# Kernel tuning notes

Hardware: AMD Instinct MI355X
Metric: run time of the kernel (lower is better)

The kernel has to match this reference:

```python
import jax, jax.numpy as jnp
import numpy as np

B, SQ, FDIM = 32, 196, 2048
L, EDIM, H = 1000, 1024, 16
DH = EDIM // H  # 64


def setup_inputs() -> dict:
    key = jax.random.key(0)
    ks = jax.random.split(key, 10)
    s = lambda fan_in: 1.0 / np.sqrt(fan_in)
    return {
        "features": jax.random.normal(ks[0], (B, SQ, FDIM), jnp.float32),
        "label_embeddings": jax.random.normal(ks[1], (L, EDIM), jnp.float32),
        "Wq": jax.random.normal(ks[2], (EDIM, FDIM), jnp.float32) * s(FDIM),
        "bq": jax.random.normal(ks[3], (EDIM,), jnp.float32) * s(FDIM),
        "Wk": jax.random.normal(ks[4], (EDIM, EDIM), jnp.float32) * s(EDIM),
        "bk": jax.random.normal(ks[5], (EDIM,), jnp.float32) * s(EDIM),
        "Wv": jax.random.normal(ks[6], (EDIM, EDIM), jnp.float32) * s(EDIM),
        "bv": jax.random.normal(ks[7], (EDIM,), jnp.float32) * s(EDIM),
        "Wo": jax.random.normal(ks[8], (EDIM, EDIM), jnp.float32) * s(EDIM),
        "bo": jax.random.normal(ks[9], (EDIM,), jnp.float32) * s(EDIM),
    }


def reference(features, label_embeddings, Wq, bq, Wk, bk, Wv, bv, Wo, bo):
    # Q projection: [B, Sq, E] -> [B, Sq, H, Dh]
    q = (jnp.einsum("bsf,ef->bse", features, Wq) + bq).reshape(B, SQ, H, DH)
    # K/V projections on the shared label table: [L, E] -> [L, H, Dh]
    k = (label_embeddings @ Wk.T + bk).reshape(L, H, DH)
    v = (label_embeddings @ Wv.T + bv).reshape(L, H, DH)
    # scores: [B, H, Sq, L]
    scores = jnp.einsum("bqhd,lhd->bhql", q, k) / jnp.sqrt(jnp.float32(DH))
    attn = jax.nn.softmax(scores, axis=-1)
    # attention output: [B, Sq, H, Dh] -> [B, Sq, E]
    ctx = jnp.einsum("bhql,lhd->bqhd", attn, v).reshape(B, SQ, EDIM)
    return jnp.einsum("bse,oe->bso", ctx, Wo) + bo
```

## Files before the change

kernel.cpp:

```cpp
#include <hip/hip_runtime.h>
#include <hip/hip_bf16.h>
#include <stdint.h>
#include <math.h>

constexpr int BB   = 32;
constexpr int SQ   = 196;
constexpr int FDIM = 2048;
constexpr int LL   = 1000;
constexpr int EDIM = 1024;
constexpr int HH   = 16;
constexpr int BSQ  = BB * SQ;

typedef unsigned short u16;
typedef unsigned int   u32;
typedef __attribute__((ext_vector_type(4)))  float f32x4;
typedef __attribute__((ext_vector_type(16))) float f32x16;
typedef __attribute__((ext_vector_type(8)))  short bf16x8;
typedef __attribute__((ext_vector_type(2)))  int   i32x2;

#define DEV __device__ __forceinline__

DEV u16 f2bf(float f) {
  unsigned u = __float_as_uint(f);
  unsigned r = 0x7FFFu + ((u >> 16) & 1u);
  return (u16)((u + r) >> 16);
}

DEV u32 pack2bf(float a, float b) {
  __hip_bfloat162 h = __float22bfloat162_rn(float2{a, b});
  return *reinterpret_cast<const u32*>(&h);
}

#if __has_builtin(__builtin_amdgcn_exp2f)
#define EXP2F(x) __builtin_amdgcn_exp2f(x)
#else
#define EXP2F(x) exp2f(x)
#endif

DEV f32x16 zero16() {
  f32x16 v;
#pragma unroll
  for (int i = 0; i < 16; ++i) v[i] = 0.f;
  return v;
}

#if __has_builtin(__builtin_amdgcn_permlane32_swap)
DEV void half_swap(u32& a, u32& b, int ) {
  i32x2 r = __builtin_amdgcn_permlane32_swap((int)a, (int)b, false, false);
  a = (u32)r[0]; b = (u32)r[1];
}
#else
DEV void half_swap(u32& a, u32& b, int hi) {
  const u32 sa = __shfl_xor(a, 32), sb = __shfl_xor(b, 32);
  const u32 na = hi ? sb : a;
  const u32 nb = hi ? b : sa;
  a = na; b = nb;
}
#endif

#define GLDS16(g, l) __builtin_amdgcn_global_load_lds(                         \
    (const __attribute__((address_space(1))) void*)(g),                       \
    (__attribute__((address_space(3))) void*)(l), 16, 0, 0)

DEV int xcd_chunk(int bid, int cpx) { return (bid & 7) * cpx + (bid >> 3); }

constexpr int C_N0 = BSQ * FDIM / 4;
constexpr int C_N1 = C_N0 + EDIM * FDIM / 4;
constexpr int C_N2 = C_N1 + EDIM * EDIM / 4;
constexpr int C_N3 = C_N2 + EDIM * EDIM / 4;
constexpr int C_N4 = C_N3 + EDIM * EDIM / 4;
constexpr int C_N5 = C_N4 + LL * EDIM / 4;

__global__ __launch_bounds__(256)
void cvt_all(const float* __restrict__ f,  const float* __restrict__ wq,
             const float* __restrict__ wk, const float* __restrict__ wv,
             const float* __restrict__ wo, const float* __restrict__ lab,
             u16* df, u16* dwq, u16* dwk, u16* dwv, u16* dwo, u16* dlab) {
  int i = blockIdx.x * blockDim.x + threadIdx.x;
  const int st = gridDim.x * blockDim.x;
  for (; i < C_N5; i += st) {
    const float* s; u16* d; int j;
    if (i < C_N0)      { s = f;   d = df;   j = i; }
    else if (i < C_N1) { s = wq;  d = dwq;  j = i - C_N0; }
    else if (i < C_N2) { s = wk;  d = dwk;  j = i - C_N1; }
    else if (i < C_N3) { s = wv;  d = dwv;  j = i - C_N2; }
    else if (i < C_N4) { s = wo;  d = dwo;  j = i - C_N3; }
    else               { s = lab; d = dlab; j = i - C_N4; }
    float4 v = reinterpret_cast<const float4*>(s)[j];
    ushort4 o;
    o.x = f2bf(v.x); o.y = f2bf(v.y); o.z = f2bf(v.z); o.w = f2bf(v.w);
    reinterpret_cast<ushort4*>(d)[j] = o;
  }
}

template<int OUTMODE>
DEV void body64(u16* sA, u16* sB, int tm, int tn,
                const u16* __restrict__ A, const u16* __restrict__ B,
                const float* __restrict__ bias, void* __restrict__ C,
                int M, int K, float scale) {
  const int lane = threadIdx.x & 63;
  const int wid  = threadIdx.x >> 6;
  const int lr = lane & 15, lg = lane >> 4;

  f32x4 acc[4][2];
#pragma unroll
  for (int m = 0; m < 4; ++m)
#pragma unroll
    for (int n = 0; n < 2; ++n) acc[m][n] = (f32x4){0.f, 0.f, 0.f, 0.f};

  for (int k0 = 0; k0 < K; k0 += 64) {
#pragma unroll
    for (int i = 0; i < 2; ++i) {
      const int chunk = wid * 2 + i;
      const int row = chunk * 8 + (lane >> 3);
      int ga = tm * 64 + row; ga = ga < M ? ga : M - 1;
      GLDS16(A + (size_t)ga * K + k0 + (lane & 7) * 8, &sA[chunk * 512]);
    }
#pragma unroll
    for (int i = 0; i < 4; ++i) {
      const int chunk = wid * 4 + i;
      const int row = chunk * 8 + (lane >> 3);
      GLDS16(B + (size_t)(tn * 128 + row) * K + k0 + (lane & 7) * 8, &sB[chunk * 512]);
    }
    asm volatile("s_waitcnt vmcnt(0)" ::: "memory");
    __syncthreads();
#pragma unroll
    for (int ks = 0; ks < 2; ++ks) {
      bf16x8 af[4], bfr[2];
#pragma unroll
      for (int m = 0; m < 4; ++m)
        af[m] = *reinterpret_cast<const bf16x8*>(&sA[(m * 16 + lr) * 64 + ks * 32 + lg * 8]);
#pragma unroll
      for (int n = 0; n < 2; ++n)
        bfr[n] = *reinterpret_cast<const bf16x8*>(&sB[(wid * 32 + n * 16 + lr) * 64 + ks * 32 + lg * 8]);
#pragma unroll
      for (int m = 0; m < 4; ++m)
#pragma unroll
        for (int n = 0; n < 2; ++n)
          acc[m][n] = __builtin_amdgcn_mfma_f32_16x16x32_bf16(af[m], bfr[n], acc[m][n], 0, 0, 0);
    }
    __syncthreads();
  }

#pragma unroll
  for (int n = 0; n < 2; ++n) {
    const int c = tn * 128 + wid * 32 + n * 16 + lr;
    const float bv = bias[c];
#pragma unroll
    for (int m = 0; m < 4; ++m) {
#pragma unroll
      for (int r = 0; r < 4; ++r) {
        const int rr = tm * 64 + m * 16 + lg * 4 + r;
        const float v = (acc[m][n][r] + bv) * scale;
        if (OUTMODE == 0)      { if (rr < M) ((u16*)C)[(size_t)rr * 1024 + c] = f2bf(v); }
        else if (OUTMODE == 1) { if (rr < M) ((float*)C)[(size_t)rr * 1024 + c] = v; }
        else                   { ((u16*)C)[(size_t)c * 1024 + rr] = (rr < M) ? f2bf(v) : (u16)0; }
      }
    }
  }
}

__global__ __launch_bounds__(256)
void gemm_qproj_kv(const u16* fA, const u16* wqb, const float* bq, u16* qo, float qscale,
                   const u16* lab, const u16* wk, const float* bk, u16* ko,
                   const u16* wv, const float* bv, u16* vto) {
  __shared__ __attribute__((aligned(16))) u16 smem[12288];
  const int bid = blockIdx.x;
  if (bid < 784) {
    const int nb = xcd_chunk(bid, 98);
    body64<0>(smem, smem + 4096, nb / 8, nb % 8, fA, wqb, bq, qo, BSQ, FDIM, qscale);
  } else {
    const int nb = xcd_chunk(bid - 784, 32);
    const int tn16 = nb % 16, tm16 = nb / 16;
    if (tn16 < 8)
      body64<0>(smem, smem + 4096, tm16, tn16, lab, wk, bk, ko, LL, EDIM, 1.0f);
    else
      body64<2>(smem, smem + 4096, tm16, tn16 - 8, lab, wv, bv, vto, LL, EDIM, 1.0f);
  }
}

__global__ __launch_bounds__(256)
void gemm_oproj(const u16* A, const u16* B, const float* bias, float* C) {
  __shared__ __attribute__((aligned(16))) u16 smem[12288];
  const int nb = xcd_chunk(blockIdx.x, 98);
  body64<1>(smem, smem + 4096, nb / 8, nb % 8, A, B, bias, C, BSQ, EDIM, 1.0f);
}

__global__ __launch_bounds__(256, 2)
void attn_kernel(const u16* __restrict__ Q, const u16* __restrict__ Kb,
                 const u16* __restrict__ VT, u16* __restrict__ ctx) {
  const int wg = xcd_chunk(blockIdx.x, 98);
  const int h = wg / 49, qb = wg % 49;
  __shared__ __attribute__((aligned(16))) u16 sm[16384];

  const int t    = threadIdx.x;
  const int lane = t & 63;
  const int wid  = t >> 6;
  const int l31  = lane & 31, hi = lane >> 5;

  const int qrow = qb * 128 + wid * 32 + l31;
  const u16* qp = Q + (size_t)qrow * EDIM + h * 64;
  bf16x8 qf[4];
#pragma unroll
  for (int ks = 0; ks < 4; ++ks)
    qf[ks] = *reinterpret_cast<const bf16x8*>(qp + ks * 16 + hi * 8);

  f32x16 ctxa[2]; ctxa[0] = zero16(); ctxa[1] = zero16();
  float lsum = 0.f;

  auto stage = [&](int buf, int l0s) {
#pragma unroll
    for (int i = 0; i < 2; ++i) {
      const int chunk = wid * 2 + i;
      const int row   = chunk * 8 + (lane >> 3);
      const int sl    = (lane & 7) ^ (row & 7);
      int lk = l0s + row; if (lk > LL - 1) lk = LL - 1;
      GLDS16(Kb + (size_t)lk * EDIM + h * 64 + sl * 8, sm + buf * 4096 + chunk * 512);
      GLDS16(VT + (size_t)(h * 64 + row) * 1024 + l0s + sl * 8, sm + 8192 + buf * 4096 + chunk * 512);
    }
  };
  auto frag = [&](const u16* base, int row, int slot) -> bf16x8 {
    return *reinterpret_cast<const bf16x8*>(base + row * 64 + ((slot ^ (row & 7)) * 8));
  };

  constexpr int NT = (LL + 63) / 64;
  stage(0, 0);
  asm volatile("s_waitcnt vmcnt(0)" ::: "memory");
  __syncthreads();

  for (int it = 0; it < NT; ++it) {
    const int l0  = it * 64;
    const int cur = it & 1;
    if (it + 1 < NT) stage(cur ^ 1, l0 + 64);

    const u16* sKb = sm + cur * 4096;
    const u16* sVb = sm + 8192 + cur * 4096;

    f32x16 st[2]; st[0] = zero16(); st[1] = zero16();
    __builtin_amdgcn_s_setprio(1);
#pragma unroll
    for (int ks = 0; ks < 4; ++ks) {
#pragma unroll
      for (int jt = 0; jt < 2; ++jt) {
        bf16x8 kf = frag(sKb, jt * 32 + l31, 2 * ks + hi);
        st[jt] = __builtin_amdgcn_mfma_f32_32x32x16_bf16(kf, qf[ks], st[jt], 0, 0, 0);
      }
    }
    __builtin_amdgcn_s_setprio(0);

    u32 pk[2][4][2];
    auto softmax_pack = [&](bool tail) {
#pragma unroll
      for (int jt = 0; jt < 2; ++jt) {
#pragma unroll
        for (int g = 0; g < 4; ++g) {
          float p[4];
#pragma unroll
          for (int j = 0; j < 4; ++j) {
            float e = EXP2F(st[jt][g * 4 + j]);
            if (tail) {
              const int kg = l0 + jt * 32 + j + 8 * g + 4 * hi;
              if (kg >= LL) e = 0.f;
            }
            p[j] = e;
            lsum += e;
          }
          pk[jt][g][0] = pack2bf(p[0], p[1]);
          pk[jt][g][1] = pack2bf(p[2], p[3]);
        }
      }
    };
    if (l0 + 64 <= LL) softmax_pack(false); else softmax_pack(true);

    __builtin_amdgcn_s_setprio(1);
#pragma unroll
    for (int ksl = 0; ksl < 4; ++ksl) {
      const int jt = ksl >> 1, e2 = ksl & 1;
      u32 x0 = pk[jt][2 * e2 + 0][0], y0 = pk[jt][2 * e2 + 1][0];
      u32 x1 = pk[jt][2 * e2 + 0][1], y1 = pk[jt][2 * e2 + 1][1];
      half_swap(x0, y0, hi);
      half_swap(x1, y1, hi);
      union { u32 d[4]; bf16x8 v; } pf;
      pf.d[0] = x0; pf.d[1] = x1; pf.d[2] = y0; pf.d[3] = y1;
#pragma unroll
      for (int dt = 0; dt < 2; ++dt) {
        bf16x8 vf = frag(sVb, dt * 32 + l31, 2 * ksl + hi);
        ctxa[dt] = __builtin_amdgcn_mfma_f32_32x32x16_bf16(vf, pf.v, ctxa[dt], 0, 0, 0);
      }
    }
    __builtin_amdgcn_s_setprio(0);

    asm volatile("s_waitcnt vmcnt(0)" ::: "memory");
    __syncthreads();
  }

  float ltot = lsum + __shfl_xor(lsum, 32);
  const float inv = 1.0f / ltot;

  u16* tb = sm;
  const int q = wid * 32 + l31;
#pragma unroll
  for (int dt = 0; dt < 2; ++dt) {
#pragma unroll
    for (int g = 0; g < 4; ++g) {
      u32 w0 = pack2bf(ctxa[dt][g * 4 + 0] * inv, ctxa[dt][g * 4 + 1] * inv);
      u32 w1 = pack2bf(ctxa[dt][g * 4 + 2] * inv, ctxa[dt][g * 4 + 3] * inv);
      const int d2   = dt * 64 + g * 16 + hi * 8;
      const int byte = q * 128 + (d2 ^ ((q & 7) << 4));
      *reinterpret_cast<u32*>(reinterpret_cast<char*>(tb) + byte)     = w0;
      *reinterpret_cast<u32*>(reinterpret_cast<char*>(tb) + byte + 4) = w1;
    }
  }
  __syncthreads();
#pragma unroll
  for (int pass = 0; pass < 4; ++pass) {
    const int row  = pass * 32 + (t >> 3);
    const int srow = qb * 128 + row;
    const int cb = ((t & 7) * 16) ^ ((row & 7) << 4);
    uint4 val = *reinterpret_cast<const uint4*>(reinterpret_cast<const char*>(tb) + row * 128 + cb);
    *reinterpret_cast<uint4*>(ctx + (size_t)srow * EDIM + h * 64 + (t & 7) * 8) = val;
  }
}

extern "C" void kernel_launch(void* const* d_in, const int* in_sizes, int n_in,
                              void* d_out, int out_size, void* d_ws, size_t ws_size,
                              hipStream_t stream) {
  const float* features = (const float*)d_in[0];
  const float* labels   = (const float*)d_in[1];
  const float* Wq = (const float*)d_in[2];
  const float* bq = (const float*)d_in[3];
  const float* Wk = (const float*)d_in[4];
  const float* bk = (const float*)d_in[5];
  const float* Wv = (const float*)d_in[6];
  const float* bv = (const float*)d_in[7];
  const float* Wo = (const float*)d_in[8];
  const float* bo = (const float*)d_in[9];
  float* out = (float*)d_out;

  u16* f_bf   = (u16*)d_ws;
  u16* wq_bf  = f_bf   + (size_t)BSQ  * FDIM;
  u16* wk_bf  = wq_bf  + (size_t)EDIM * FDIM;
  u16* wv_bf  = wk_bf  + (size_t)EDIM * EDIM;
  u16* wo_bf  = wv_bf  + (size_t)EDIM * EDIM;
  u16* lab_bf = wo_bf  + (size_t)EDIM * EDIM;
  u16* q_bf   = lab_bf + (size_t)LL   * EDIM;
  u16* k_bf   = q_bf   + (size_t)BSQ  * EDIM;
  u16* vt_bf  = k_bf   + (size_t)LL   * EDIM;
  u16* ctx_bf = vt_bf  + (size_t)1024 * 1024;

  cvt_all<<<2048, 256, 0, stream>>>(features, Wq, Wk, Wv, Wo, labels,
                                    f_bf, wq_bf, wk_bf, wv_bf, wo_bf, lab_bf);

  const float qscale = 0.125f * 1.4426950408889634f;
  gemm_qproj_kv<<<784 + 256, 256, 0, stream>>>(
      f_bf, wq_bf, bq, q_bf, qscale,
      lab_bf, wk_bf, bk, k_bf, wv_bf, bv, vt_bf);

  attn_kernel<<<784, 256, 0, stream>>>(q_bf, k_bf, vt_bf, ctx_bf);

  gemm_oproj<<<784, 256, 0, stream>>>(ctx_bf, wo_bf, bo, out);
}
```

Before: 158.4 us.

## Double-buffer LDS in projection GEMMs to overlap global loads with MFMA

Doubles the shared memory tile buffers in the shared GEMM body so the global-to-LDS copies for tile k+2 are issued while tile k is being computed. A partial vmcnt wait replaces the full wait, so one stage of loads stays in flight across iterations. Each iteration now has two barriers instead of one, and LDS use per block doubles to 48KB, which may lower occupancy.

```diff
diff --git a/kernel.cpp b/kernel.cpp
--- a/kernel.cpp
+++ b/kernel.cpp
@@ -94,7 +94,7 @@
 }
 
 template<int OUTMODE>
-DEV void body64(u16* sA, u16* sB, int tm, int tn,
+DEV void body64(u16* sAb, u16* sBb, int tm, int tn,
                 const u16* __restrict__ A, const u16* __restrict__ B,
                 const float* __restrict__ bias, void* __restrict__ C,
                 int M, int K, float scale) {
@@ -108,38 +108,60 @@
 #pragma unroll
     for (int n = 0; n < 2; ++n) acc[m][n] = (f32x4){0.f, 0.f, 0.f, 0.f};
 
-  for (int k0 = 0; k0 < K; k0 += 64) {
+  auto stage = [&](int buf, int k0) {
 #pragma unroll
     for (int i = 0; i < 2; ++i) {
       const int chunk = wid * 2 + i;
       const int row = chunk * 8 + (lane >> 3);
       int ga = tm * 64 + row; ga = ga < M ? ga : M - 1;
-      GLDS16(A + (size_t)ga * K + k0 + (lane & 7) * 8, &sA[chunk * 512]);
+      GLDS16(A + (size_t)ga * K + k0 + (lane & 7) * 8, &sAb[buf * 4096 + chunk * 512]);
     }
 #pragma unroll
     for (int i = 0; i < 4; ++i) {
       const int chunk = wid * 4 + i;
       const int row = chunk * 8 + (lane >> 3);
-      GLDS16(B + (size_t)(tn * 128 + row) * K + k0 + (lane & 7) * 8, &sB[chunk * 512]);
-    }
-    asm volatile("s_waitcnt vmcnt(0)" ::: "memory");
-    __syncthreads();
+      GLDS16(B + (size_t)(tn * 128 + row) * K + k0 + (lane & 7) * 8, &sBb[buf * 8192 + chunk * 512]);
+    }
+  };
+
+  const int NK = K >> 6;
+  stage(0, 0);
+  stage(1, 64);
+  asm volatile("s_waitcnt vmcnt(6)" ::: "memory");
+  __builtin_amdgcn_sched_barrier(0);
+  __builtin_amdgcn_s_barrier();
+  __builtin_amdgcn_sched_barrier(0);
+
+  for (int t = 0; t < NK; ++t) {
+    const u16* pA = sAb + (t & 1) * 4096;
+    const u16* pB = sBb + (t & 1) * 8192;
 #pragma unroll
     for (int ks = 0; ks < 2; ++ks) {
       bf16x8 af[4], bfr[2];
 #pragma unroll
       for (int m = 0; m < 4; ++m)
-        af[m] = *reinterpret_cast<const bf16x8*>(&sA[(m * 16 + lr) * 64 + ks * 32 + lg * 8]);
+        af[m] = *reinterpret_cast<const bf16x8*>(&pA[(m * 16 + lr) * 64 + ks * 32 + lg * 8]);
 #pragma unroll
       for (int n = 0; n < 2; ++n)
-        bfr[n] = *reinterpret_cast<const bf16x8*>(&sB[(wid * 32 + n * 16 + lr) * 64 + ks * 32 + lg * 8]);
+        bfr[n] = *reinterpret_cast<const bf16x8*>(&pB[(wid * 32 + n * 16 + lr) * 64 + ks * 32 + lg * 8]);
 #pragma unroll
       for (int m = 0; m < 4; ++m)
 #pragma unroll
         for (int n = 0; n < 2; ++n)
           acc[m][n] = __builtin_amdgcn_mfma_f32_16x16x32_bf16(af[m], bfr[n], acc[m][n], 0, 0, 0);
     }
-    __syncthreads();
+    __builtin_amdgcn_sched_barrier(0);
+    __builtin_amdgcn_s_barrier();
+    __builtin_amdgcn_sched_barrier(0);
+    if (t + 2 < NK) {
+      stage(t & 1, (t + 2) << 6);
+      asm volatile("s_waitcnt vmcnt(6)" ::: "memory");
+    } else {
+      asm volatile("s_waitcnt vmcnt(0)" ::: "memory");
+    }
+    __builtin_amdgcn_sched_barrier(0);
+    __builtin_amdgcn_s_barrier();
+    __builtin_amdgcn_sched_barrier(0);
   }
 
 #pragma unroll
@@ -164,26 +186,26 @@
 void gemm_qproj_kv(const u16* fA, const u16* wqb, const float* bq, u16* qo, float qscale,
                    const u16* lab, const u16* wk, const float* bk, u16* ko,
                    const u16* wv, const float* bv, u16* vto) {
-  __shared__ __attribute__((aligned(16))) u16 smem[12288];
+  __shared__ __attribute__((aligned(16))) u16 smem[24576];
   const int bid = blockIdx.x;
   if (bid < 784) {
     const int nb = xcd_chunk(bid, 98);
-    body64<0>(smem, smem + 4096, nb / 8, nb % 8, fA, wqb, bq, qo, BSQ, FDIM, qscale);
+    body64<0>(smem, smem + 8192, nb / 8, nb % 8, fA, wqb, bq, qo, BSQ, FDIM, qscale);
   } else {
     const int nb = xcd_chunk(bid - 784, 32);
     const int tn16 = nb % 16, tm16 = nb / 16;
     if (tn16 < 8)
-      body64<0>(smem, smem + 4096, tm16, tn16, lab, wk, bk, ko, LL, EDIM, 1.0f);
+      body64<0>(smem, smem + 8192, tm16, tn16, lab, wk, bk, ko, LL, EDIM, 1.0f);
     else
-      body64<2>(smem, smem + 4096, tm16, tn16 - 8, lab, wv, bv, vto, LL, EDIM, 1.0f);
+      body64<2>(smem, smem + 8192, tm16, tn16 - 8, lab, wv, bv, vto, LL, EDIM, 1.0f);
   }
 }
 
 __global__ __launch_bounds__(256)
 void gemm_oproj(const u16* A, const u16* B, const float* bias, float* C) {
-  __shared__ __attribute__((aligned(16))) u16 smem[12288];
+  __shared__ __attribute__((aligned(16))) u16 smem[24576];
   const int nb = xcd_chunk(blockIdx.x, 98);
-  body64<1>(smem, smem + 4096, nb / 8, nb % 8, A, B, bias, C, BSQ, EDIM, 1.0f);
+  body64<1>(smem, smem + 8192, nb / 8, nb % 8, A, B, bias, C, BSQ, EDIM, 1.0f);
 }
 
 __global__ __launch_bounds__(256, 2)
```

Result: no change. 158.7 us (+0.2%).
